# Kernel optimization log

Hardware: AMD Instinct MI355X
Metric: run time of the kernel (lower is better)

Reference implementation:

```python
import jax, jax.numpy as jnp
import numpy as np

N_USERS = 40000
N_ITEMS = 60000
N_NODES = N_USERS + N_ITEMS
EMBED_DIM = 64
NNZ = 1_200_000
BATCH = 1024
NEG_SLOPE = 0.2
EPS = 1e-12


def setup_inputs() -> dict:
    key = jax.random.key(0)
    ks = jax.random.split(key, 12)
    s = 1.0 / np.sqrt(EMBED_DIM)  # xavier-ish scale
    inp = {
        "user_embed": jax.random.normal(ks[0], (N_USERS, EMBED_DIM), jnp.float32) * s,
        "item_embed": jax.random.normal(ks[1], (N_ITEMS, EMBED_DIM), jnp.float32) * s,
        "W1_0": jax.random.normal(ks[2], (EMBED_DIM, EMBED_DIM), jnp.float32) * s,
        "W1_1": jax.random.normal(ks[3], (EMBED_DIM, EMBED_DIM), jnp.float32) * s,
        "W1_2": jax.random.normal(ks[4], (EMBED_DIM, EMBED_DIM), jnp.float32) * s,
        "W2_0": jax.random.normal(ks[5], (EMBED_DIM, EMBED_DIM), jnp.float32) * s,
        "W2_1": jax.random.normal(ks[6], (EMBED_DIM, EMBED_DIM), jnp.float32) * s,
        "W2_2": jax.random.normal(ks[7], (EMBED_DIM, EMBED_DIM), jnp.float32) * s,
        "adj_vals": jax.random.uniform(ks[8], (NNZ,), jnp.float32),
        "adj_rows": jax.random.randint(ks[9], (NNZ,), 0, N_NODES, jnp.int32),
        "adj_cols": jax.random.randint(ks[10], (NNZ,), 0, N_NODES, jnp.int32),
        "user_ids": jax.random.randint(ks[11], (BATCH,), 0, N_USERS, jnp.int32),
        "item_ids": jax.random.randint(jax.random.fold_in(key, 99), (BATCH,), 0, N_ITEMS, jnp.int32),
    }
    return inp


def _l2_normalize(x):
    # torch F.normalize(p=2, dim=1): x / max(||x||, eps)
    n = jnp.sqrt(jnp.sum(x * x, axis=1, keepdims=True))
    return x / jnp.maximum(n, EPS)


def _propagate(user_embed, item_embed, W1s, W2s, adj_vals, adj_rows, adj_cols):
    E = jnp.concatenate([user_embed, item_embed], axis=0)  # [N, d]
    layer_embs = [E]
    for W1, W2 in zip(W1s, W2s):
        # sparse adjacency SpMM: E_gc[r] = sum_e vals[e] * E[cols[e]] for rows[e]==r
        msgs = adj_vals[:, None] * E[adj_cols]  # [nnz, d]
        E_gc = jax.ops.segment_sum(msgs, adj_rows, num_segments=N_NODES)
        side1 = (E + E_gc) @ W1  # Linear(bias=False); W stored [in, out]
        side2 = (E_gc * E) @ W2
        E = jax.nn.leaky_relu(side1 + side2, NEG_SLOPE)
        E = _l2_normalize(E)  # eval mode: dropout skipped
        layer_embs.append(E)
    E_all = jnp.concatenate(layer_embs, axis=1)  # [N, 4*d]
    return E_all[:N_USERS], E_all[N_USERS:]


def reference(user_embed, item_embed, W1_0, W1_1, W1_2, W2_0, W2_1, W2_2,
              adj_vals, adj_rows, adj_cols, user_ids, item_ids):
    u_emb, i_emb = _propagate(user_embed, item_embed,
                              (W1_0, W1_1, W1_2), (W2_0, W2_1, W2_2),
                              adj_vals, adj_rows, adj_cols)
    u = u_emb[user_ids]  # [B, 4d]
    i = i_emb[item_ids]  # [B, 4d]
    return u @ i.T  # [B, B] scores
```

## Files before the change

kernel.cpp:

```cpp
#include <hip/hip_runtime.h>
#include <hip/hip_bf16.h>
#include <hip/hip_fp16.h>

#define N_USERS 40000
#define N_ITEMS 60000
#define N_NODES 100000
#define NPAD 100032
#define DIM 64
#define NNZ 1200000
#define BATCH 1024
#define NEG_SLOPE 0.2f
#define NPART 8
#define PROWS ((N_NODES + NPART - 1) / NPART)

typedef _Float16 half8 __attribute__((ext_vector_type(8)));
typedef float f32x4 __attribute__((ext_vector_type(4)));


__global__ void k_zero(int* __restrict__ p, int n) {
    int i = blockIdx.x * blockDim.x + threadIdx.x;
    if (i < n) p[i] = 0;
}

__global__ __launch_bounds__(256) void k_count(const int* __restrict__ rows,
                                               int* __restrict__ counts) {
    int p = blockIdx.x & (NPART - 1);
    int chunk = blockIdx.x >> 3;
    int nchunk = gridDim.x >> 3;
    int per = (NNZ + nchunk - 1) / nchunk;
    int lo = chunk * per;
    int hi = min(lo + per, NNZ);
    int rlo = p * PROWS, rhi = rlo + PROWS;
    for (int e = lo + (int)threadIdx.x; e < hi; e += 256) {
        int r = rows[e];
        if (r >= rlo && r < rhi) atomicAdd(&counts[r], 1);
    }
}

__global__ void k_scanA(const int* __restrict__ counts, int* __restrict__ blk) {
    __shared__ int s[256];
    int base = blockIdx.x * 1024;
    int t = threadIdx.x;
    int sum = 0;
#pragma unroll
    for (int j = 0; j < 4; j++) {
        int i = base + t * 4 + j;
        if (i < N_NODES) sum += counts[i];
    }
    s[t] = sum;
    __syncthreads();
    for (int off = 128; off > 0; off >>= 1) {
        if (t < off) s[t] += s[t + off];
        __syncthreads();
    }
    if (t == 0) blk[blockIdx.x] = s[0];
}

__global__ void k_scanB(int* __restrict__ blk, int nblk, int* __restrict__ row_ptr) {
    __shared__ int s[128];
    int t = threadIdx.x;
    int v = (t < nblk) ? blk[t] : 0;
    s[t] = v;
    __syncthreads();
    for (int off = 1; off < 128; off <<= 1) {
        int x = (t >= off) ? s[t - off] : 0;
        __syncthreads();
        s[t] += x;
        __syncthreads();
    }
    if (t < nblk) blk[t] = s[t] - v;
    if (t == 0) row_ptr[N_NODES] = s[nblk - 1];
}

__global__ void k_scanC(const int* __restrict__ counts, const int* __restrict__ blk,
                        int* __restrict__ row_ptr, int* __restrict__ cursors) {
    __shared__ int s[256];
    int base = blockIdx.x * 1024;
    int t = threadIdx.x;
    int local[4];
    int sum = 0;
#pragma unroll
    for (int j = 0; j < 4; j++) {
        int i = base + t * 4 + j;
        int v = (i < N_NODES) ? counts[i] : 0;
        local[j] = v;
        sum += v;
    }
    s[t] = sum;
    __syncthreads();
    for (int off = 1; off < 256; off <<= 1) {
        int v2 = (t >= off) ? s[t - off] : 0;
        __syncthreads();
        s[t] += v2;
        __syncthreads();
    }
    int excl = s[t] - sum + blk[blockIdx.x];
#pragma unroll
    for (int j = 0; j < 4; j++) {
        int i = base + t * 4 + j;
        if (i < N_NODES) {
            row_ptr[i] = excl;
            cursors[i] = excl;
            excl += local[j];
        }
    }
}

__global__ __launch_bounds__(256) void k_scatter(const int* __restrict__ rows,
                                                 const int* __restrict__ cols,
                                                 const float* __restrict__ vals,
                                                 int* __restrict__ cursors,
                                                 int2* __restrict__ edges) {
    int p = blockIdx.x & (NPART - 1);
    int chunk = blockIdx.x >> 3;
    int nchunk = gridDim.x >> 3;
    int per = (NNZ + nchunk - 1) / nchunk;
    int lo = chunk * per;
    int hi = min(lo + per, NNZ);
    int rlo = p * PROWS, rhi = rlo + PROWS;
    for (int e = lo + (int)threadIdx.x; e < hi; e += 256) {
        int r = rows[e];
        if (r >= rlo && r < rhi) {
            int pos = atomicAdd(&cursors[r], 1);
            edges[pos] = make_int2(cols[e], __float_as_int(vals[e]));
        }
    }
}


__global__ void k_initE(const float4* __restrict__ ue, const float4* __restrict__ ie,
                        float4* __restrict__ E, __half2* __restrict__ Eh2) {
    int i = blockIdx.x * blockDim.x + threadIdx.x;
    const int UQ = N_USERS * DIM / 4;
    const int TQ = N_NODES * DIM / 4;
    float4 v;
    if (i < UQ) v = ue[i];
    else if (i < TQ) v = ie[i - UQ];
    else return;
    E[i] = v;
    Eh2[i * 2] = __floats2half2_rn(v.x, v.y);
    Eh2[i * 2 + 1] = __floats2half2_rn(v.z, v.w);
}

__global__ __launch_bounds__(256) void k_spmm(const __half2* __restrict__ Eh2,
                                              const int* __restrict__ rp,
                                              const int2* __restrict__ edges,
                                              float* __restrict__ Egc) {
    int gid = blockIdx.x * blockDim.x + threadIdx.x;
    int r = gid >> 6, lane = gid & 63;
    if (r >= N_NODES) return;
    int half = lane >> 5, l32 = lane & 31;
    int s = rp[r], e = rp[r + 1];
    float2 acc = make_float2(0.f, 0.f);
    int j = s;
    for (; j + 8 <= e; j += 8) {
        int base = j + half * 4;
        int2 q0 = edges[base], q1 = edges[base + 1], q2 = edges[base + 2], q3 = edges[base + 3];
        float2 f0 = __half22float2(Eh2[(size_t)q0.x * 32 + l32]);
        float2 f1 = __half22float2(Eh2[(size_t)q1.x * 32 + l32]);
        float2 f2 = __half22float2(Eh2[(size_t)q2.x * 32 + l32]);
        float2 f3 = __half22float2(Eh2[(size_t)q3.x * 32 + l32]);
        float v0 = __int_as_float(q0.y), v1 = __int_as_float(q1.y);
        float v2 = __int_as_float(q2.y), v3 = __int_as_float(q3.y);
        acc.x = fmaf(v0, f0.x, acc.x); acc.y = fmaf(v0, f0.y, acc.y);
        acc.x = fmaf(v1, f1.x, acc.x); acc.y = fmaf(v1, f1.y, acc.y);
        acc.x = fmaf(v2, f2.x, acc.x); acc.y = fmaf(v2, f2.y, acc.y);
        acc.x = fmaf(v3, f3.x, acc.x); acc.y = fmaf(v3, f3.y, acc.y);
    }
    for (; j + 2 <= e; j += 2) {
        int2 q = edges[j + half];
        float2 f = __half22float2(Eh2[(size_t)q.x * 32 + l32]);
        float v = __int_as_float(q.y);
        acc.x = fmaf(v, f.x, acc.x);
        acc.y = fmaf(v, f.y, acc.y);
    }
    if (j < e && half == 0) {
        int2 q = edges[j];
        float2 f = __half22float2(Eh2[(size_t)q.x * 32 + l32]);
        float v = __int_as_float(q.y);
        acc.x = fmaf(v, f.x, acc.x);
        acc.y = fmaf(v, f.y, acc.y);
    }
    acc.x += __shfl_xor(acc.x, 32);
    acc.y += __shfl_xor(acc.y, 32);
    if (half == 0) *(float2*)&Egc[(size_t)r * DIM + l32 * 2] = acc;
}

__global__ __launch_bounds__(256) void k_xform(float* __restrict__ E,
                                               const float* __restrict__ G,
                                               __half* __restrict__ Eh,
                                               const float* __restrict__ W1,
                                               const float* __restrict__ W2) {
    int l = threadIdx.x & 63;
    int wv = threadIdx.x >> 6;
    int m = l & 15;
    int ko = (l >> 4) * 8;

    half8 b1[4][2], b2[4][2];
#pragma unroll
    for (int t = 0; t < 4; t++)
#pragma unroll
        for (int c = 0; c < 2; c++)
#pragma unroll
            for (int jj = 0; jj < 8; jj++) {
                int k = c * 32 + ko + jj;
                b1[t][c][jj] = (_Float16)W1[k * DIM + t * 16 + m];
                b2[t][c][jj] = (_Float16)W2[k * DIM + t * 16 + m];
            }

    size_t base = (size_t)blockIdx.x * 64 + wv * 16;

    half8 a1[2], a2[2];
#pragma unroll
    for (int c = 0; c < 2; c++) {
        const float* pe = &E[(base + m) * DIM + c * 32 + ko];
        const float* pg = &G[(base + m) * DIM + c * 32 + ko];
        float4 e0 = *(const float4*)pe, e1 = *(const float4*)(pe + 4);
        float4 g0 = *(const float4*)pg, g1 = *(const float4*)(pg + 4);
        a1[c][0] = (_Float16)(e0.x + g0.x); a2[c][0] = (_Float16)(e0.x * g0.x);
        a1[c][1] = (_Float16)(e0.y + g0.y); a2[c][1] = (_Float16)(e0.y * g0.y);
        a1[c][2] = (_Float16)(e0.z + g0.z); a2[c][2] = (_Float16)(e0.z * g0.z);
        a1[c][3] = (_Float16)(e0.w + g0.w); a2[c][3] = (_Float16)(e0.w * g0.w);
        a1[c][4] = (_Float16)(e1.x + g1.x); a2[c][4] = (_Float16)(e1.x * g1.x);
        a1[c][5] = (_Float16)(e1.y + g1.y); a2[c][5] = (_Float16)(e1.y * g1.y);
        a1[c][6] = (_Float16)(e1.z + g1.z); a2[c][6] = (_Float16)(e1.z * g1.z);
        a1[c][7] = (_Float16)(e1.w + g1.w); a2[c][7] = (_Float16)(e1.w * g1.w);
    }

    f32x4 acc[4];
#pragma unroll
    for (int t = 0; t < 4; t++) {
        acc[t] = (f32x4){0.f, 0.f, 0.f, 0.f};
        acc[t] = __builtin_amdgcn_mfma_f32_16x16x32_f16(a1[0], b1[t][0], acc[t], 0, 0, 0);
        acc[t] = __builtin_amdgcn_mfma_f32_16x16x32_f16(a1[1], b1[t][1], acc[t], 0, 0, 0);
        acc[t] = __builtin_amdgcn_mfma_f32_16x16x32_f16(a2[0], b2[t][0], acc[t], 0, 0, 0);
        acc[t] = __builtin_amdgcn_mfma_f32_16x16x32_f16(a2[1], b2[t][1], acc[t], 0, 0, 0);
    }

    float vv[4][4];
    float part[4];
#pragma unroll
    for (int q = 0; q < 4; q++) part[q] = 0.f;
#pragma unroll
    for (int t = 0; t < 4; t++)
#pragma unroll
        for (int q = 0; q < 4; q++) {
            float v = acc[t][q];
            v = v > 0.f ? v : NEG_SLOPE * v;
            vv[t][q] = v;
            part[q] = fmaf(v, v, part[q]);
        }
#pragma unroll
    for (int q = 0; q < 4; q++) {
#pragma unroll
        for (int off = 1; off < 16; off <<= 1) part[q] += __shfl_xor(part[q], off);
        part[q] = fmaxf(sqrtf(part[q]), 1e-12f);
    }
#pragma unroll
    for (int t = 0; t < 4; t++)
#pragma unroll
        for (int q = 0; q < 4; q++) {
            float o = vv[t][q] / part[q];
            size_t row = base + (l >> 4) * 4 + q;
            E[row * DIM + t * 16 + m] = o;
            Eh[row * DIM + t * 16 + m] = __float2half(o);
        }
}

__global__ void k_gather(const float* __restrict__ E, const int* __restrict__ uids,
                         const int* __restrict__ iids, float* __restrict__ uf,
                         float* __restrict__ inf, int col0) {
    int gid = blockIdx.x * blockDim.x + threadIdx.x;
    int row = gid >> 6, lane = gid & 63;
    if (row < BATCH) {
        uf[row * 256 + col0 + lane] = E[(size_t)uids[row] * DIM + lane];
    } else if (row < 2 * BATCH) {
        int r = row - BATCH;
        inf[r * 256 + col0 + lane] = E[(size_t)(N_USERS + iids[r]) * DIM + lane];
    }
}


__global__ __launch_bounds__(256) void k_score(const float* __restrict__ uf,
                                               const float* __restrict__ inf,
                                               float* __restrict__ out) {
    __shared__ float su[32][68];
    __shared__ float si[32][68];
    int t = threadIdx.x;
    int bx = blockIdx.x & 15, by = blockIdx.x >> 4;
    int tx = t & 15, ty = t >> 4;
    int lrow = t >> 2;
    int lk = (t & 3) * 8;
    float acc[4][4] = {};
    for (int kk = 0; kk < 256; kk += 32) {
        float4 a0 = *(const float4*)&uf[(by * 64 + lrow) * 256 + kk + lk];
        float4 a1 = *(const float4*)&uf[(by * 64 + lrow) * 256 + kk + lk + 4];
        float4 b0 = *(const float4*)&inf[(bx * 64 + lrow) * 256 + kk + lk];
        float4 b1 = *(const float4*)&inf[(bx * 64 + lrow) * 256 + kk + lk + 4];
        __syncthreads();
        su[lk + 0][lrow] = a0.x; su[lk + 1][lrow] = a0.y;
        su[lk + 2][lrow] = a0.z; su[lk + 3][lrow] = a0.w;
        su[lk + 4][lrow] = a1.x; su[lk + 5][lrow] = a1.y;
        su[lk + 6][lrow] = a1.z; su[lk + 7][lrow] = a1.w;
        si[lk + 0][lrow] = b0.x; si[lk + 1][lrow] = b0.y;
        si[lk + 2][lrow] = b0.z; si[lk + 3][lrow] = b0.w;
        si[lk + 4][lrow] = b1.x; si[lk + 5][lrow] = b1.y;
        si[lk + 6][lrow] = b1.z; si[lk + 7][lrow] = b1.w;
        __syncthreads();
#pragma unroll
        for (int k = 0; k < 32; k++) {
            const float* pu = &su[k][ty * 4];
            const float* pi = &si[k][tx * 4];
#pragma unroll
            for (int mi = 0; mi < 4; mi++)
#pragma unroll
                for (int ni = 0; ni < 4; ni++)
                    acc[mi][ni] = fmaf(pu[mi], pi[ni], acc[mi][ni]);
        }
    }
#pragma unroll
    for (int mi = 0; mi < 4; mi++)
#pragma unroll
        for (int ni = 0; ni < 4; ni++)
            out[(size_t)(by * 64 + ty * 4 + mi) * 1024 + bx * 64 + tx * 4 + ni] = acc[mi][ni];
}


extern "C" void kernel_launch(void* const* d_in, const int* in_sizes, int n_in,
                              void* d_out, int out_size, void* d_ws, size_t ws_size,
                              hipStream_t stream) {
    const float* user_embed = (const float*)d_in[0];
    const float* item_embed = (const float*)d_in[1];
    const float* W1[3] = {(const float*)d_in[2], (const float*)d_in[3], (const float*)d_in[4]};
    const float* W2[3] = {(const float*)d_in[5], (const float*)d_in[6], (const float*)d_in[7]};
    const float* adj_vals = (const float*)d_in[8];
    const int* adj_rows = (const int*)d_in[9];
    const int* adj_cols = (const int*)d_in[10];
    const int* user_ids = (const int*)d_in[11];
    const int* item_ids = (const int*)d_in[12];
    float* out = (float*)d_out;

    float* E = (float*)d_ws;
    float* Egc = E + (size_t)NPAD * DIM;
    __half* Eh = (__half*)(Egc + (size_t)NPAD * DIM);
    float* uf = (float*)(Eh + (size_t)NPAD * DIM);
    float* inf = uf + BATCH * 256;
    int2* edges = (int2*)(inf + BATCH * 256);
    int* row_ptr = (int*)(edges + NNZ);
    int* cursors = row_ptr + (N_NODES + 1);
    int* counts = cursors + N_NODES;
    int* blk = counts + N_NODES;

    const int NBLK = (N_NODES + 1023) / 1024;

    k_zero<<<(N_NODES + 255) / 256, 256, 0, stream>>>(counts, N_NODES);
    k_count<<<1024, 256, 0, stream>>>(adj_rows, counts);
    k_scanA<<<NBLK, 256, 0, stream>>>(counts, blk);
    k_scanB<<<1, 128, 0, stream>>>(blk, NBLK, row_ptr);
    k_scanC<<<NBLK, 256, 0, stream>>>(counts, blk, row_ptr, cursors);
    k_scatter<<<1024, 256, 0, stream>>>(adj_rows, adj_cols, adj_vals, cursors, edges);

    k_initE<<<(N_NODES * DIM / 4 + 255) / 256, 256, 0, stream>>>(
        (const float4*)user_embed, (const float4*)item_embed, (float4*)E, (__half2*)Eh);
    k_gather<<<(2 * BATCH * DIM) / 256, 256, 0, stream>>>(E, user_ids, item_ids, uf, inf, 0);

    for (int l = 0; l < 3; l++) {
        k_spmm<<<(N_NODES * DIM) / 256, 256, 0, stream>>>((const __half2*)Eh, row_ptr, edges, Egc);
        k_xform<<<NPAD / 64, 256, 0, stream>>>(E, Egc, Eh, W1[l], W2[l]);
        k_gather<<<(2 * BATCH * DIM) / 256, 256, 0, stream>>>(E, user_ids, item_ids, uf, inf,
                                                              (l + 1) * 64);
    }

    k_score<<<256, 256, 0, stream>>>(uf, inf, out);
}
```

Before: 434.9 us.

## Fuse SpMM into layer transform kernel and simplify CSR build with per-edge positions

Merges the per-layer SpMM and dense transform into one kernel. Each block computes the aggregated neighbor sums for its 64 rows into shared memory and then applies the MFMA transform, which removes the Egc global round trip and one launch per layer. The half-precision embedding is double-buffered so the gather reads never race with the writes. The CSR build is also rewritten: the partitioned count/scatter is replaced by a single atomic pass that records each edge's position, plus a scatter without atomics. The risk is lower SpMM parallelism, since each wave now processes 16 rows serially inside a block, and the unpartitioned atomics have less locality.

```diff
diff --git a/kernel.cpp b/kernel.cpp
--- a/kernel.cpp
+++ b/kernel.cpp
@@ -10,8 +10,6 @@
 #define NNZ 1200000
 #define BATCH 1024
 #define NEG_SLOPE 0.2f
-#define NPART 8
-#define PROWS ((N_NODES + NPART - 1) / NPART)
 
 typedef _Float16 half8 __attribute__((ext_vector_type(8)));
 typedef float f32x4 __attribute__((ext_vector_type(4)));
@@ -22,19 +20,10 @@
     if (i < n) p[i] = 0;
 }
 
-__global__ __launch_bounds__(256) void k_count(const int* __restrict__ rows,
-                                               int* __restrict__ counts) {
-    int p = blockIdx.x & (NPART - 1);
-    int chunk = blockIdx.x >> 3;
-    int nchunk = gridDim.x >> 3;
-    int per = (NNZ + nchunk - 1) / nchunk;
-    int lo = chunk * per;
-    int hi = min(lo + per, NNZ);
-    int rlo = p * PROWS, rhi = rlo + PROWS;
-    for (int e = lo + (int)threadIdx.x; e < hi; e += 256) {
-        int r = rows[e];
-        if (r >= rlo && r < rhi) atomicAdd(&counts[r], 1);
-    }
+__global__ void k_count(const int* __restrict__ rows, int* __restrict__ counts,
+                        int* __restrict__ pos) {
+    int e = blockIdx.x * blockDim.x + threadIdx.x;
+    if (e < NNZ) pos[e] = atomicAdd(&counts[rows[e]], 1);
 }
 
 __global__ void k_scanA(const int* __restrict__ counts, int* __restrict__ blk) {
@@ -73,7 +62,7 @@
 }
 
 __global__ void k_scanC(const int* __restrict__ counts, const int* __restrict__ blk,
-                        int* __restrict__ row_ptr, int* __restrict__ cursors) {
+                        int* __restrict__ row_ptr) {
     __shared__ int s[256];
     int base = blockIdx.x * 1024;
     int t = threadIdx.x;
@@ -100,30 +89,18 @@
         int i = base + t * 4 + j;
         if (i < N_NODES) {
             row_ptr[i] = excl;
-            cursors[i] = excl;
             excl += local[j];
         }
     }
 }
 
-__global__ __launch_bounds__(256) void k_scatter(const int* __restrict__ rows,
-                                                 const int* __restrict__ cols,
-                                                 const float* __restrict__ vals,
-                                                 int* __restrict__ cursors,
-                                                 int2* __restrict__ edges) {
-    int p = blockIdx.x & (NPART - 1);
-    int chunk = blockIdx.x >> 3;
-    int nchunk = gridDim.x >> 3;
-    int per = (NNZ + nchunk - 1) / nchunk;
-    int lo = chunk * per;
-    int hi = min(lo + per, NNZ);
-    int rlo = p * PROWS, rhi = rlo + PROWS;
-    for (int e = lo + (int)threadIdx.x; e < hi; e += 256) {
-        int r = rows[e];
-        if (r >= rlo && r < rhi) {
-            int pos = atomicAdd(&cursors[r], 1);
-            edges[pos] = make_int2(cols[e], __float_as_int(vals[e]));
-        }
+__global__ void k_scatter(const int* __restrict__ rows, const int* __restrict__ cols,
+                          const float* __restrict__ vals, const int* __restrict__ rp,
+                          const int* __restrict__ pos, int2* __restrict__ edges) {
+    int e = blockIdx.x * blockDim.x + threadIdx.x;
+    if (e < NNZ) {
+        int slot = rp[rows[e]] + pos[e];
+        edges[slot] = make_int2(cols[e], __float_as_int(vals[e]));
     }
 }
 
@@ -142,81 +119,84 @@
     Eh2[i * 2 + 1] = __floats2half2_rn(v.z, v.w);
 }
 
-__global__ __launch_bounds__(256) void k_spmm(const __half2* __restrict__ Eh2,
-                                              const int* __restrict__ rp,
-                                              const int2* __restrict__ edges,
-                                              float* __restrict__ Egc) {
-    int gid = blockIdx.x * blockDim.x + threadIdx.x;
-    int r = gid >> 6, lane = gid & 63;
-    if (r >= N_NODES) return;
-    int half = lane >> 5, l32 = lane & 31;
-    int s = rp[r], e = rp[r + 1];
-    float2 acc = make_float2(0.f, 0.f);
-    int j = s;
-    for (; j + 8 <= e; j += 8) {
-        int base = j + half * 4;
-        int2 q0 = edges[base], q1 = edges[base + 1], q2 = edges[base + 2], q3 = edges[base + 3];
-        float2 f0 = __half22float2(Eh2[(size_t)q0.x * 32 + l32]);
-        float2 f1 = __half22float2(Eh2[(size_t)q1.x * 32 + l32]);
-        float2 f2 = __half22float2(Eh2[(size_t)q2.x * 32 + l32]);
-        float2 f3 = __half22float2(Eh2[(size_t)q3.x * 32 + l32]);
-        float v0 = __int_as_float(q0.y), v1 = __int_as_float(q1.y);
-        float v2 = __int_as_float(q2.y), v3 = __int_as_float(q3.y);
-        acc.x = fmaf(v0, f0.x, acc.x); acc.y = fmaf(v0, f0.y, acc.y);
-        acc.x = fmaf(v1, f1.x, acc.x); acc.y = fmaf(v1, f1.y, acc.y);
-        acc.x = fmaf(v2, f2.x, acc.x); acc.y = fmaf(v2, f2.y, acc.y);
-        acc.x = fmaf(v3, f3.x, acc.x); acc.y = fmaf(v3, f3.y, acc.y);
-    }
-    for (; j + 2 <= e; j += 2) {
-        int2 q = edges[j + half];
-        float2 f = __half22float2(Eh2[(size_t)q.x * 32 + l32]);
-        float v = __int_as_float(q.y);
-        acc.x = fmaf(v, f.x, acc.x);
-        acc.y = fmaf(v, f.y, acc.y);
-    }
-    if (j < e && half == 0) {
-        int2 q = edges[j];
-        float2 f = __half22float2(Eh2[(size_t)q.x * 32 + l32]);
-        float v = __int_as_float(q.y);
-        acc.x = fmaf(v, f.x, acc.x);
-        acc.y = fmaf(v, f.y, acc.y);
-    }
-    acc.x += __shfl_xor(acc.x, 32);
-    acc.y += __shfl_xor(acc.y, 32);
-    if (half == 0) *(float2*)&Egc[(size_t)r * DIM + l32 * 2] = acc;
-}
-
-__global__ __launch_bounds__(256) void k_xform(float* __restrict__ E,
-                                               const float* __restrict__ G,
-                                               __half* __restrict__ Eh,
+__global__ __launch_bounds__(256) void k_layer(const __half2* __restrict__ Eh_in,
+                                               const int* __restrict__ rp,
+                                               const int2* __restrict__ edges,
+                                               float* __restrict__ E,
+                                               __half* __restrict__ Eh_out,
                                                const float* __restrict__ W1,
                                                const float* __restrict__ W2) {
-    int l = threadIdx.x & 63;
-    int wv = threadIdx.x >> 6;
+    __shared__ float gs[64][68];
+    int t = threadIdx.x;
+    int l = t & 63, w = t >> 6;
+    int half = l >> 5, l32 = l & 31;
+    int base = blockIdx.x * 64;
+
+    for (int i = 0; i < 16; i++) {
+        int r = base + w * 16 + i;
+        float2 acc = make_float2(0.f, 0.f);
+        if (r < N_NODES) {
+            int s = rp[r], e = rp[r + 1];
+            int j = s;
+            for (; j + 8 <= e; j += 8) {
+                int eb = j + half * 4;
+                int2 q0 = edges[eb], q1 = edges[eb + 1], q2 = edges[eb + 2], q3 = edges[eb + 3];
+                float2 f0 = __half22float2(Eh_in[(size_t)q0.x * 32 + l32]);
+                float2 f1 = __half22float2(Eh_in[(size_t)q1.x * 32 + l32]);
+                float2 f2 = __half22float2(Eh_in[(size_t)q2.x * 32 + l32]);
+                float2 f3 = __half22float2(Eh_in[(size_t)q3.x * 32 + l32]);
+                float v0 = __int_as_float(q0.y), v1 = __int_as_float(q1.y);
+                float v2 = __int_as_float(q2.y), v3 = __int_as_float(q3.y);
+                acc.x = fmaf(v0, f0.x, acc.x); acc.y = fmaf(v0, f0.y, acc.y);
+                acc.x = fmaf(v1, f1.x, acc.x); acc.y = fmaf(v1, f1.y, acc.y);
+                acc.x = fmaf(v2, f2.x, acc.x); acc.y = fmaf(v2, f2.y, acc.y);
+                acc.x = fmaf(v3, f3.x, acc.x); acc.y = fmaf(v3, f3.y, acc.y);
+            }
+            for (; j + 2 <= e; j += 2) {
+                int2 q = edges[j + half];
+                float2 f = __half22float2(Eh_in[(size_t)q.x * 32 + l32]);
+                float v = __int_as_float(q.y);
+                acc.x = fmaf(v, f.x, acc.x);
+                acc.y = fmaf(v, f.y, acc.y);
+            }
+            if (j < e && half == 0) {
+                int2 q = edges[j];
+                float2 f = __half22float2(Eh_in[(size_t)q.x * 32 + l32]);
+                float v = __int_as_float(q.y);
+                acc.x = fmaf(v, f.x, acc.x);
+                acc.y = fmaf(v, f.y, acc.y);
+            }
+        }
+        acc.x += __shfl_xor(acc.x, 32);
+        acc.y += __shfl_xor(acc.y, 32);
+        if (half == 0) *(float2*)&gs[w * 16 + i][l32 * 2] = acc;
+    }
+
+    __builtin_amdgcn_sched_barrier(0);
+
     int m = l & 15;
     int ko = (l >> 4) * 8;
 
     half8 b1[4][2], b2[4][2];
 #pragma unroll
-    for (int t = 0; t < 4; t++)
+    for (int tt = 0; tt < 4; tt++)
 #pragma unroll
         for (int c = 0; c < 2; c++)
 #pragma unroll
             for (int jj = 0; jj < 8; jj++) {
                 int k = c * 32 + ko + jj;
-                b1[t][c][jj] = (_Float16)W1[k * DIM + t * 16 + m];
-                b2[t][c][jj] = (_Float16)W2[k * DIM + t * 16 + m];
+                b1[tt][c][jj] = (_Float16)W1[k * DIM + tt * 16 + m];
+                b2[tt][c][jj] = (_Float16)W2[k * DIM + tt * 16 + m];
             }
 
-    size_t base = (size_t)blockIdx.x * 64 + wv * 16;
-
+    size_t rowm = (size_t)base + w * 16 + m;
     half8 a1[2], a2[2];
 #pragma unroll
     for (int c = 0; c < 2; c++) {
-        const float* pe = &E[(base + m) * DIM + c * 32 + ko];
-        const float* pg = &G[(base + m) * DIM + c * 32 + ko];
+        const float* pe = &E[rowm * DIM + c * 32 + ko];
         float4 e0 = *(const float4*)pe, e1 = *(const float4*)(pe + 4);
-        float4 g0 = *(const float4*)pg, g1 = *(const float4*)(pg + 4);
+        float4 g0 = *(const float4*)&gs[w * 16 + m][c * 32 + ko];
+        float4 g1 = *(const float4*)&gs[w * 16 + m][c * 32 + ko + 4];
         a1[c][0] = (_Float16)(e0.x + g0.x); a2[c][0] = (_Float16)(e0.x * g0.x);
         a1[c][1] = (_Float16)(e0.y + g0.y); a2[c][1] = (_Float16)(e0.y * g0.y);
         a1[c][2] = (_Float16)(e0.z + g0.z); a2[c][2] = (_Float16)(e0.z * g0.z);
@@ -229,12 +209,12 @@
 
     f32x4 acc[4];
 #pragma unroll
-    for (int t = 0; t < 4; t++) {
-        acc[t] = (f32x4){0.f, 0.f, 0.f, 0.f};
-        acc[t] = __builtin_amdgcn_mfma_f32_16x16x32_f16(a1[0], b1[t][0], acc[t], 0, 0, 0);
-        acc[t] = __builtin_amdgcn_mfma_f32_16x16x32_f16(a1[1], b1[t][1], acc[t], 0, 0, 0);
-        acc[t] = __builtin_amdgcn_mfma_f32_16x16x32_f16(a2[0], b2[t][0], acc[t], 0, 0, 0);
-        acc[t] = __builtin_amdgcn_mfma_f32_16x16x32_f16(a2[1], b2[t][1], acc[t], 0, 0, 0);
+    for (int tt = 0; tt < 4; tt++) {
+        acc[tt] = (f32x4){0.f, 0.f, 0.f, 0.f};
+        acc[tt] = __builtin_amdgcn_mfma_f32_16x16x32_f16(a1[0], b1[tt][0], acc[tt], 0, 0, 0);
+        acc[tt] = __builtin_amdgcn_mfma_f32_16x16x32_f16(a1[1], b1[tt][1], acc[tt], 0, 0, 0);
+        acc[tt] = __builtin_amdgcn_mfma_f32_16x16x32_f16(a2[0], b2[tt][0], acc[tt], 0, 0, 0);
+        acc[tt] = __builtin_amdgcn_mfma_f32_16x16x32_f16(a2[1], b2[tt][1], acc[tt], 0, 0, 0);
     }
 
     float vv[4][4];
@@ -242,12 +222,12 @@
 #pragma unroll
     for (int q = 0; q < 4; q++) part[q] = 0.f;
 #pragma unroll
-    for (int t = 0; t < 4; t++)
+    for (int tt = 0; tt < 4; tt++)
 #pragma unroll
         for (int q = 0; q < 4; q++) {
-            float v = acc[t][q];
+            float v = acc[tt][q];
             v = v > 0.f ? v : NEG_SLOPE * v;
-            vv[t][q] = v;
+            vv[tt][q] = v;
             part[q] = fmaf(v, v, part[q]);
         }
 #pragma unroll
@@ -257,13 +237,13 @@
         part[q] = fmaxf(sqrtf(part[q]), 1e-12f);
     }
 #pragma unroll
-    for (int t = 0; t < 4; t++)
+    for (int tt = 0; tt < 4; tt++)
 #pragma unroll
         for (int q = 0; q < 4; q++) {
-            float o = vv[t][q] / part[q];
-            size_t row = base + (l >> 4) * 4 + q;
-            E[row * DIM + t * 16 + m] = o;
-            Eh[row * DIM + t * 16 + m] = __float2half(o);
+            float o = vv[tt][q] / part[q];
+            size_t row = (size_t)base + w * 16 + (l >> 4) * 4 + q;
+            E[row * DIM + tt * 16 + m] = o;
+            Eh_out[row * DIM + tt * 16 + m] = __float2half(o);
         }
 }
 
@@ -341,32 +321,34 @@
     float* out = (float*)d_out;
 
     float* E = (float*)d_ws;
-    float* Egc = E + (size_t)NPAD * DIM;
-    __half* Eh = (__half*)(Egc + (size_t)NPAD * DIM);
-    float* uf = (float*)(Eh + (size_t)NPAD * DIM);
+    __half* Eh0 = (__half*)(E + (size_t)NPAD * DIM);
+    __half* Eh1 = Eh0 + (size_t)NPAD * DIM;
+    float* uf = (float*)(Eh1 + (size_t)NPAD * DIM);
     float* inf = uf + BATCH * 256;
     int2* edges = (int2*)(inf + BATCH * 256);
-    int* row_ptr = (int*)(edges + NNZ);
-    int* cursors = row_ptr + (N_NODES + 1);
-    int* counts = cursors + N_NODES;
+    int* pos = (int*)(edges + NNZ);
+    int* row_ptr = pos + NNZ;
+    int* counts = row_ptr + (N_NODES + 1);
     int* blk = counts + N_NODES;
 
     const int NBLK = (N_NODES + 1023) / 1024;
 
     k_zero<<<(N_NODES + 255) / 256, 256, 0, stream>>>(counts, N_NODES);
-    k_count<<<1024, 256, 0, stream>>>(adj_rows, counts);
+    k_count<<<(NNZ + 255) / 256, 256, 0, stream>>>(adj_rows, counts, pos);
     k_scanA<<<NBLK, 256, 0, stream>>>(counts, blk);
     k_scanB<<<1, 128, 0, stream>>>(blk, NBLK, row_ptr);
-    k_scanC<<<NBLK, 256, 0, stream>>>(counts, blk, row_ptr, cursors);
-    k_scatter<<<1024, 256, 0, stream>>>(adj_rows, adj_cols, adj_vals, cursors, edges);
+    k_scanC<<<NBLK, 256, 0, stream>>>(counts, blk, row_ptr);
+    k_scatter<<<(NNZ + 255) / 256, 256, 0, stream>>>(adj_rows, adj_cols, adj_vals,
+                                                     row_ptr, pos, edges);
 
     k_initE<<<(N_NODES * DIM / 4 + 255) / 256, 256, 0, stream>>>(
-        (const float4*)user_embed, (const float4*)item_embed, (float4*)E, (__half2*)Eh);
+        (const float4*)user_embed, (const float4*)item_embed, (float4*)E, (__half2*)Eh0);
     k_gather<<<(2 * BATCH * DIM) / 256, 256, 0, stream>>>(E, user_ids, item_ids, uf, inf, 0);
 
+    __half* hb[2] = {Eh0, Eh1};
     for (int l = 0; l < 3; l++) {
-        k_spmm<<<(N_NODES * DIM) / 256, 256, 0, stream>>>((const __half2*)Eh, row_ptr, edges, Egc);
-        k_xform<<<NPAD / 64, 256, 0, stream>>>(E, Egc, Eh, W1[l], W2[l]);
+        k_layer<<<NPAD / 64, 256, 0, stream>>>((const __half2*)hb[l & 1], row_ptr, edges,
+                                               E, hb[(l + 1) & 1], W1[l], W2[l]);
         k_gather<<<(2 * BATCH * DIM) / 256, 256, 0, stream>>>(E, user_ids, item_ids, uf, inf,
                                                               (l + 1) * 64);
     }
```

Result: slower. 477.5 us (+9.8%).
